# Optimization experiments

Measured on AMD Instinct MI355X. Metric: run time of the kernel, lower is better.

The kernel has to match this reference:

```python
import jax, jax.numpy as jnp
import numpy as np

D_MODEL = 1024
N_HEADS = 16
D_K = D_MODEL // N_HEADS  # 64
D_FF = 2688
THETA = 10000.0
EPS = 1e-5
B, S = 2, 2048


def _rmsnorm(x, w):
    xf = x.astype(jnp.float32)
    ms = jnp.mean(xf * xf, axis=-1, keepdims=True)
    return (xf * w * jax.lax.rsqrt(ms + EPS)).astype(x.dtype)


def _rope(x, cos, sin):
    # x: [B, S, H, D_K]; cos/sin: [S, D_K//2]
    xe = x[..., 0::2]
    xo = x[..., 1::2]
    c = cos[None, :, None, :]
    s = sin[None, :, None, :]
    re = xe * c - xo * s
    ro = xe * s + xo * c
    # interleave back to even/odd layout
    return jnp.stack([re, ro], axis=-1).reshape(x.shape)


def setup_inputs() -> dict:
    key = jax.random.key(0)
    ks = jax.random.split(key, 12)
    sc = 0.02  # keep activations numerically sane (stand-in for trunc_normal init)
    return {
        "x": jax.random.normal(ks[0], (B, S, D_MODEL), dtype=jnp.float32),
        "ln1_w": jax.random.normal(ks[1], (D_MODEL,), dtype=jnp.float32) * sc + 1.0,
        "q_w": jax.random.normal(ks[2], (D_MODEL, D_MODEL), dtype=jnp.float32) * sc,
        "k_w": jax.random.normal(ks[3], (D_MODEL, D_MODEL), dtype=jnp.float32) * sc,
        "v_w": jax.random.normal(ks[4], (D_MODEL, D_MODEL), dtype=jnp.float32) * sc,
        "o_w": jax.random.normal(ks[5], (D_MODEL, D_MODEL), dtype=jnp.float32) * sc,
        "ln2_w": jax.random.normal(ks[6], (D_MODEL,), dtype=jnp.float32) * sc + 1.0,
        "w1_w": jax.random.normal(ks[7], (D_FF, D_MODEL), dtype=jnp.float32) * sc,
        "w3_w": jax.random.normal(ks[8], (D_FF, D_MODEL), dtype=jnp.float32) * sc,
        "w2_w": jax.random.normal(ks[9], (D_MODEL, D_FF), dtype=jnp.float32) * sc,
        "token_positions": jnp.arange(S, dtype=jnp.int32),
    }


def reference(x, ln1_w, q_w, k_w, v_w, o_w, ln2_w, w1_w, w3_w, w2_w, token_positions):
    b, s, _ = x.shape
    # --- pre-norm attention sublayer ---
    h = _rmsnorm(x, ln1_w)
    Q = (h @ q_w.T).reshape(b, s, N_HEADS, D_K)
    K = (h @ k_w.T).reshape(b, s, N_HEADS, D_K)
    V = (h @ v_w.T).reshape(b, s, N_HEADS, D_K)

    # RoPE tables from token positions
    pos = token_positions.astype(jnp.float32)                      # [S]
    kk = jnp.arange(D_K // 2, dtype=jnp.float32)
    inv_freq = THETA ** (-2.0 * kk / D_K)                          # [D_K/2]
    ang = pos[:, None] * inv_freq[None, :]                          # [S, D_K/2]
    cos, sin = jnp.cos(ang), jnp.sin(ang)

    Qr = _rope(Q, cos, sin)
    Kr = _rope(K, cos, sin)

    scale = 1.0 / jnp.sqrt(jnp.float32(D_K))
    scores = jnp.einsum("bqhd,bkhd->bhqk", Qr, Kr) * scale          # [B,H,S,S]
    causal = jnp.tril(jnp.ones((s, s), dtype=bool))
    scores = jnp.where(causal[None, None], scores, jnp.float32(-10000.0))
    attn = jax.nn.softmax(scores, axis=-1)
    ctx = jnp.einsum("bhqk,bkhd->bqhd", attn, V).reshape(b, s, D_MODEL)
    x1 = x + ctx @ o_w.T

    # --- pre-norm SwiGLU FFN sublayer ---
    h2 = _rmsnorm(x1, ln2_w)
    g = h2 @ w1_w.T                                                 # [B,S,D_FF]
    u = h2 @ w3_w.T
    ffn = (g * jax.nn.sigmoid(g) * u) @ w2_w.T
    return x1 + ffn
```

## Files before the change

kernel.cpp:

```cpp
#include <hip/hip_runtime.h>
#include <cstdint>

#define DM   1024
#define NH   16
#define DK   64
#define DFF  2688
#define SEQ  2048
#define BB   2
#define MTOT (BB*SEQ)

typedef __attribute__((ext_vector_type(8))) short short8;
typedef __attribute__((ext_vector_type(4))) float f32x4;

typedef const __attribute__((address_space(1))) void* gaddr_t;
typedef __attribute__((address_space(3))) void* laddr_t;
#define GLOAD_LDS16(g, l) __builtin_amdgcn_global_load_lds((gaddr_t)(g), (laddr_t)(l), 16, 0, 0)
#define MFMA16(a, b, c) __builtin_amdgcn_mfma_f32_16x16x32_bf16((a), (b), (c), 0, 0, 0)
#define WAIT_LDS() __builtin_amdgcn_s_waitcnt(0xc07f)

#define VMCNT(n) asm volatile("s_waitcnt vmcnt(" #n ")" ::: "memory")
#define BAR() do { asm volatile("" ::: "memory"); \
                   __builtin_amdgcn_s_barrier();  \
                   asm volatile("" ::: "memory"); } while (0)

__device__ __forceinline__ float bf2f(unsigned short u) {
    union { unsigned int i; float f; } v; v.i = ((unsigned int)u) << 16; return v.f;
}
__device__ __forceinline__ unsigned short f2bf(float f) {
    union { float f; unsigned int i; } v; v.f = f;
    unsigned int r = v.i + 0x7fffu + ((v.i >> 16) & 1u);
    return (unsigned short)(r >> 16);
}
__device__ __forceinline__ unsigned long long pack4bf(float a, float b, float c, float d) {
    return (unsigned long long)f2bf(a) | ((unsigned long long)f2bf(b) << 16)
         | ((unsigned long long)f2bf(c) << 32) | ((unsigned long long)f2bf(d) << 48);
}

__global__ __launch_bounds__(256)
void prologue_k(const float* __restrict__ q_w, const float* __restrict__ k_w,
                const float* __restrict__ v_w, const float* __restrict__ o_w,
                const float* __restrict__ w1_w, const float* __restrict__ w3_w,
                const float* __restrict__ w2_w,
                unsigned short* __restrict__ Wqkv, unsigned short* __restrict__ Wo,
                unsigned short* __restrict__ W13, unsigned short* __restrict__ W2,
                const int* __restrict__ pos, float* __restrict__ tab,
                const float* __restrict__ x, const float* __restrict__ ln1_w,
                unsigned short* __restrict__ H) {
    const int blk = blockIdx.x;
    const int tid = threadIdx.x;
    if (blk < 12160) {
        const float* src; unsigned short* dst; int cols, rmul, roff, i;
        if (blk < 4096) {
            const int rr = blk >> 10;
            i = (blk & 1023) * 256 + tid;
            cols = 1024; rmul = 1;
            if (rr == 0)      { src = q_w; dst = Wqkv; roff = 0; }
            else if (rr == 1) { src = k_w; dst = Wqkv; roff = 1024; }
            else if (rr == 2) { src = v_w; dst = Wqkv; roff = 2048; }
            else              { src = o_w; dst = Wo;   roff = 0; }
        } else if (blk < 6784) {
            i = (blk - 4096) * 256 + tid; src = w1_w; dst = W13; cols = 1024; rmul = 2; roff = 0;
        } else if (blk < 9472) {
            i = (blk - 6784) * 256 + tid; src = w3_w; dst = W13; cols = 1024; rmul = 2; roff = 1;
        } else {
            i = (blk - 9472) * 256 + tid; src = w2_w; dst = W2;  cols = 2688; rmul = 1; roff = 0;
        }
        const int e = i * 4;
        const int r = e / cols, c = e - r * cols;
        const float4 v = *(const float4*)(src + e);
        ushort4 o;
        o.x = f2bf(v.x); o.y = f2bf(v.y); o.z = f2bf(v.z); o.w = f2bf(v.w);
        *(ushort4*)(dst + (size_t)(r * rmul + roff) * cols + c) = o;
    } else if (blk < 12672) {
        const int s = (blk - 12160) * 4 + (tid >> 6);
        const int t = tid & 63;
        const int kk = t & 31;
        const float ang = (float)pos[s] * __expf(-0.28782313662f * (float)kk);
        tab[s * 64 + t] = (t < 32) ? cosf(ang) : sinf(ang);
    } else {
        const int row = blk - 12672;
        const float4 v = ((const float4*)(x + (size_t)row * DM))[tid];
        float ss = v.x * v.x + v.y * v.y + v.z * v.z + v.w * v.w;
#pragma unroll
        for (int off = 32; off > 0; off >>= 1) ss += __shfl_down(ss, off, 64);
        __shared__ float sred[4];
        const int wave = tid >> 6, lane = tid & 63;
        if (lane == 0) sred[wave] = ss;
        __syncthreads();
        const float tot = sred[0] + sred[1] + sred[2] + sred[3];
        const float rinv = rsqrtf(tot * (1.0f / DM) + 1e-5f);
        const float4 wv = ((const float4*)ln1_w)[tid];
        ushort4 o;
        o.x = f2bf(v.x * wv.x * rinv);
        o.y = f2bf(v.y * wv.y * rinv);
        o.z = f2bf(v.z * wv.z * rinv);
        o.w = f2bf(v.w * wv.w * rinv);
        ((ushort4*)(H + (size_t)row * DM))[tid] = o;
    }
}

__global__ __launch_bounds__(256)
void rmsnorm_k(const float* __restrict__ x, const float* __restrict__ w,
               unsigned short* __restrict__ out) {
    const int row = blockIdx.x;
    const int tid = threadIdx.x;
    const float4 v = ((const float4*)(x + (size_t)row * DM))[tid];
    float ss = v.x * v.x + v.y * v.y + v.z * v.z + v.w * v.w;
#pragma unroll
    for (int off = 32; off > 0; off >>= 1) ss += __shfl_down(ss, off, 64);
    __shared__ float sred[4];
    const int wave = tid >> 6, lane = tid & 63;
    if (lane == 0) sred[wave] = ss;
    __syncthreads();
    const float tot = sred[0] + sred[1] + sred[2] + sred[3];
    const float rinv = rsqrtf(tot * (1.0f / DM) + 1e-5f);
    const float4 wv = ((const float4*)w)[tid];
    ushort4 o;
    o.x = f2bf(v.x * wv.x * rinv);
    o.y = f2bf(v.y * wv.y * rinv);
    o.z = f2bf(v.z * wv.z * rinv);
    o.w = f2bf(v.w * wv.w * rinv);
    ((ushort4*)(out + (size_t)row * DM))[tid] = o;
}

template <int EPI>
__global__ __launch_bounds__(512)
void gemm256(const unsigned short* __restrict__ A,
             const unsigned short* __restrict__ B,
             unsigned short* __restrict__ O0,
             unsigned short* __restrict__ O1,
             unsigned short* __restrict__ O2,
             const float* __restrict__ ROPT,
             int N, int K) {
    __shared__ unsigned short As[2][16384];
    __shared__ unsigned short Bs[2][12288];
    const int tid = threadIdx.x;
    const int wave = tid >> 6, lane = tid & 63;
    const int l15 = lane & 15, quad = lane >> 4;

    const int gx = gridDim.x;
    const int nwg = gx * gridDim.y;
    const int lin = blockIdx.y * gx + blockIdx.x;
    const int swz = (lin & 7) * (nwg >> 3) + (lin >> 3);
    const int bx = swz % gx, by = swz / gx;
    const int m0 = by * 256, n0 = bx * 192;
    const int wr = (wave >> 2) * 128, wc = (wave & 3) * 48;

    const f32x4 z4 = {0.f, 0.f, 0.f, 0.f};
    f32x4 acc[8][3];
#pragma unroll
    for (int m = 0; m < 8; m++)
#pragma unroll
        for (int n = 0; n < 3; n++) acc[m][n] = z4;

    const unsigned short* pa[4];
    int la[4];
#pragma unroll
    for (int r = 0; r < 4; r++) {
        const int s = r * 512 + tid;
        pa[r] = A + (size_t)(m0 + (s & 255)) * K + (s >> 8) * 8;
        la[r] = (r * 512 + wave * 64) * 8;
    }
    const unsigned short* pb[3];
    int lb[3];
#pragma unroll
    for (int r = 0; r < 3; r++) {
        const int s = r * 512 + tid;
        const int bk = s / 192, br = s - bk * 192;
        pb[r] = B + (size_t)(n0 + br) * K + bk * 8;
        lb[r] = (r * 512 + wave * 64) * 8;
    }

    const int nt = K >> 6;

#pragma unroll
    for (int r = 0; r < 4; r++) { GLOAD_LDS16(pa[r], &As[0][la[r]]); pa[r] += 64; }
#pragma unroll
    for (int r = 0; r < 3; r++) { GLOAD_LDS16(pb[r], &Bs[0][lb[r]]); pb[r] += 64; }

    int cur = 0;
    for (int t = 0; t < nt; ++t) {
        const int nb = cur ^ 1;
        if (t + 1 < nt) {
#pragma unroll
            for (int r = 0; r < 4; r++) { GLOAD_LDS16(pa[r], &As[nb][la[r]]); pa[r] += 64; }
            VMCNT(4);
        } else {
            VMCNT(0);
        }
        BAR();

        short8 bg[3][2];
#pragma unroll
        for (int n = 0; n < 3; n++)
#pragma unroll
            for (int kk = 0; kk < 2; kk++)
                bg[n][kk] = *(const short8*)(&Bs[cur][((quad + 4 * kk) * 192 + wc + n * 16 + l15) * 8]);

        short8 afA[2][2], afB[2][2];
#pragma unroll
        for (int m = 0; m < 2; m++)
#pragma unroll
            for (int kk = 0; kk < 2; kk++)
                afA[m][kk] = *(const short8*)(&As[cur][((quad + 4 * kk) * 256 + wr + m * 16 + l15) * 8]);

#pragma unroll
        for (int p = 0; p < 4; ++p) {
            short8 (&afC)[2][2] = (p & 1) ? afB : afA;
            short8 (&afN)[2][2] = (p & 1) ? afA : afB;
            if (p < 3) {
#pragma unroll
                for (int m = 0; m < 2; m++)
#pragma unroll
                    for (int kk = 0; kk < 2; kk++)
                        afN[m][kk] = *(const short8*)(&As[cur][((quad + 4 * kk) * 256 + wr + ((p + 1) * 2 + m) * 16 + l15) * 8]);
            }
            if (p == 1 && t + 1 < nt) {
#pragma unroll
                for (int r = 0; r < 3; r++) { GLOAD_LDS16(pb[r], &Bs[nb][lb[r]]); pb[r] += 64; }
            }
            __builtin_amdgcn_s_setprio(1);
#pragma unroll
            for (int m = 0; m < 2; m++)
#pragma unroll
                for (int n = 0; n < 3; n++)
#pragma unroll
                    for (int kk = 0; kk < 2; kk++)
                        acc[p * 2 + m][n] = MFMA16(bg[n][kk], afC[m][kk], acc[p * 2 + m][n]);
            __builtin_amdgcn_s_setprio(0);
            BAR();
        }
        cur = nb;
    }

#pragma unroll
    for (int m = 0; m < 8; m++) {
        const int r = m0 + wr + m * 16 + l15;
        if (EPI == 0) {
            const int b = r >> 11, s = r & (SEQ - 1);
            const float* rt = ROPT + s * 64;
#pragma unroll
            for (int n = 0; n < 3; n++) {
                const int cb = n0 + wc + n * 16;
                const int sec = cb >> 10;
                const int h = (cb & 1023) >> 6;
                const int cc0 = (cb & 63) + quad * 4;
                const f32x4 a = acc[m][n];
                if (sec < 2) {
                    const int p0 = cc0 >> 1;
                    const float cA = rt[p0],     sA = rt[32 + p0];
                    const float cB = rt[p0 + 1], sB = rt[32 + p0 + 1];
                    const float e0 = a[0] * cA - a[1] * sA;
                    const float o0 = a[0] * sA + a[1] * cA;
                    const float e1 = a[2] * cB - a[3] * sB;
                    const float o1 = a[2] * sB + a[3] * cB;
                    unsigned short* dst = (sec == 0) ? O0 : O1;
                    *(unsigned long long*)(dst + ((size_t)(b * NH + h) * SEQ + s) * DK + cc0) =
                        pack4bf(e0, o0, e1, o1);
                } else {
                    unsigned short* dst = O2 + ((size_t)(b * NH + h) * DK) * SEQ + s;
#pragma unroll
                    for (int tq = 0; tq < 4; tq++)
                        dst[(size_t)(cc0 + tq) * SEQ] = f2bf(a[tq]);
                }
            }
        } else {
#pragma unroll
            for (int n = 0; n < 3; n++) {
                const int cc = n0 + wc + n * 16 + quad * 4;
                const f32x4 a = acc[m][n];
                const float s1 = a[0] * a[1] / (1.f + __expf(-a[0]));
                const float s2 = a[2] * a[3] / (1.f + __expf(-a[2]));
                *(unsigned int*)(O0 + (size_t)r * (DFF) + (cc >> 1)) =
                    (unsigned int)f2bf(s1) | ((unsigned int)f2bf(s2) << 16);
            }
        }
    }
}

__global__ __launch_bounds__(512)
void gemm_thin(const unsigned short* __restrict__ A,
               const unsigned short* __restrict__ B,
               float* __restrict__ Cf,
               const float* __restrict__ R,
               int N, int K) {
    __shared__ unsigned short As[2][8192];
    __shared__ unsigned short Bs[2][8192];
    const int tid = threadIdx.x;
    const int wave = tid >> 6, lane = tid & 63;
    const int l15 = lane & 15, quad = lane >> 4;

    const int gx = gridDim.x;
    const int nwg = gx * gridDim.y;
    const int lin = blockIdx.y * gx + blockIdx.x;
    const int swz = (lin & 7) * (nwg >> 3) + (lin >> 3);
    const int bx = swz % gx, by = swz / gx;
    const int m0 = by * 128, n0 = bx * 128;
    const int wr = (wave >> 2) * 64, wc = (wave & 3) * 32;

    const f32x4 z4 = {0.f, 0.f, 0.f, 0.f};
    f32x4 acc[4][2];
#pragma unroll
    for (int m = 0; m < 4; m++)
#pragma unroll
        for (int n = 0; n < 2; n++) acc[m][n] = z4;

    const unsigned short* pa[2];
    const unsigned short* pb[2];
    int la[2], lb[2];
#pragma unroll
    for (int r = 0; r < 2; r++) {
        const int s = r * 512 + tid;
        pa[r] = A + (size_t)(m0 + (s & 127)) * K + (s >> 7) * 8;
        pb[r] = B + (size_t)(n0 + (s & 127)) * K + (s >> 7) * 8;
        la[r] = (r * 512 + wave * 64) * 8;
        lb[r] = la[r];
    }

    const int nt = K >> 6;

#pragma unroll
    for (int r = 0; r < 2; r++) { GLOAD_LDS16(pa[r], &As[0][la[r]]); pa[r] += 64; }
#pragma unroll
    for (int r = 0; r < 2; r++) { GLOAD_LDS16(pb[r], &Bs[0][lb[r]]); pb[r] += 64; }

    int cur = 0;
    for (int t = 0; t < nt; ++t) {
        const int nb = cur ^ 1;
        if (t + 1 < nt) {
#pragma unroll
            for (int r = 0; r < 2; r++) { GLOAD_LDS16(pa[r], &As[nb][la[r]]); pa[r] += 64; }
            VMCNT(2);
        } else {
            VMCNT(0);
        }
        BAR();

        short8 bg[2][2];
#pragma unroll
        for (int n = 0; n < 2; n++)
#pragma unroll
            for (int kk = 0; kk < 2; kk++)
                bg[n][kk] = *(const short8*)(&Bs[cur][((quad + 4 * kk) * 128 + wc + n * 16 + l15) * 8]);

#pragma unroll
        for (int p = 0; p < 2; ++p) {
            if (p == 0 && t + 1 < nt) {
#pragma unroll
                for (int r = 0; r < 2; r++) { GLOAD_LDS16(pb[r], &Bs[nb][lb[r]]); pb[r] += 64; }
            }
            short8 af[2][2];
#pragma unroll
            for (int m = 0; m < 2; m++)
#pragma unroll
                for (int kk = 0; kk < 2; kk++)
                    af[m][kk] = *(const short8*)(&As[cur][((quad + 4 * kk) * 128 + wr + (p * 2 + m) * 16 + l15) * 8]);
            __builtin_amdgcn_s_setprio(1);
#pragma unroll
            for (int m = 0; m < 2; m++)
#pragma unroll
                for (int n = 0; n < 2; n++)
#pragma unroll
                    for (int kk = 0; kk < 2; kk++)
                        acc[p * 2 + m][n] = MFMA16(bg[n][kk], af[m][kk], acc[p * 2 + m][n]);
            __builtin_amdgcn_s_setprio(0);
            BAR();
        }
        cur = nb;
    }

#pragma unroll
    for (int i = 0; i < 4; i++) {
        const int r = m0 + wr + i * 16 + l15;
#pragma unroll
        for (int j = 0; j < 2; j++) {
            const int cc = n0 + wc + j * 16 + quad * 4;
            const size_t idx = (size_t)r * N + cc;
            const float4 rv = *(const float4*)(R + idx);
            float4 ov;
            ov.x = acc[i][j][0] + rv.x;
            ov.y = acc[i][j][1] + rv.y;
            ov.z = acc[i][j][2] + rv.z;
            ov.w = acc[i][j][3] + rv.w;
            *(float4*)(Cf + idx) = ov;
        }
    }
}

template <bool MASK>
__device__ __forceinline__ void softmax_tile(f32x4 st[4], float& li, unsigned short* Pw,
                                             int l15, int quad, int j0, int myq) {
    float lsum = 0.f;
#pragma unroll
    for (int t = 0; t < 4; t++) {
#pragma unroll
        for (int r = 0; r < 4; r++) {
            float v = st[t][r] * 0.125f;
            if (MASK) {
                const int key = j0 + t * 16 + quad * 4 + r;
                if (key > myq) v = -1e30f;
            }
            const float p = __expf(v);
            st[t][r] = p;
            lsum += p;
        }
        *(unsigned long long*)(Pw + l15 * 72 + t * 16 + quad * 4) =
            pack4bf(st[t][0], st[t][1], st[t][2], st[t][3]);
    }
    li += lsum;
}

__global__ __launch_bounds__(256, 2)
void attn_k(const unsigned short* __restrict__ Qr, const unsigned short* __restrict__ Kr,
            const unsigned short* __restrict__ Vt, unsigned short* __restrict__ ctx) {
    __shared__ unsigned short KVl[2][8192];
    __shared__ unsigned short Pl[4 * 2 * 1152];
    const int tid = threadIdx.x;
    const int wave = tid >> 6, lane = tid & 63;
    const int l15 = lane & 15, quad = lane >> 4;
    const int bh = blockIdx.y, b = bh >> 4, h = bh & 15;
    const int g = blockIdx.x;
    const int qtA = g * 4 + wave, qtB = 127 - qtA;
    const int q0A = qtA * 16, q0B = qtB * 16;
    const int countA = g + 1, countB = 32 - g;
    const unsigned short* Kb = Kr + (size_t)bh * SEQ * DK;
    const unsigned short* Vb = Vt + (size_t)bh * DK * SEQ;

    const unsigned short* QbA = Qr + ((size_t)bh * SEQ + q0A) * DK;
    const unsigned short* QbB = Qr + ((size_t)bh * SEQ + q0B) * DK;
    const short8 qfA0 = *(const short8*)(QbA + l15 * DK + quad * 8);
    const short8 qfA1 = *(const short8*)(QbA + l15 * DK + 32 + quad * 8);
    const short8 qfB0 = *(const short8*)(QbB + l15 * DK + quad * 8);
    const short8 qfB1 = *(const short8*)(QbB + l15 * DK + 32 + quad * 8);

    const int slot0 = wave * 128 + lane, slot1 = slot0 + 64;
    const int ck0 = slot0 >> 3, s0 = slot0 & 7;
    const int ck1 = slot1 >> 3, s1 = slot1 & 7;
    const unsigned short* kp0 = Kb + ck0 * 64 + (s0 ^ (ck0 & 7)) * 8;
    const unsigned short* kp1 = Kb + ck1 * 64 + (s1 ^ (ck1 & 7)) * 8;
    const unsigned short* vp0 = Vb + ck0 * 2048 + (s0 ^ (ck0 & 7)) * 8;
    const unsigned short* vp1 = Vb + ck1 * 2048 + (s1 ^ (ck1 & 7)) * 8;
    const int kb0 = wave * 1024, kb1 = kb0 + 512;

    unsigned short* PA = Pl + (wave * 2 + 0) * 1152;
    unsigned short* PB = Pl + (wave * 2 + 1) * 1152;

    const f32x4 z4 = {0.f, 0.f, 0.f, 0.f};
    f32x4 oA[4], oB[4];
#pragma unroll
    for (int d = 0; d < 4; d++) { oA[d] = z4; oB[d] = z4; }
    float liA = 0.f, liB = 0.f;
    const int myqA = q0A + l15, myqB = q0B + l15;
    const int xr = l15 & 7;

    GLOAD_LDS16(kp0, &KVl[0][kb0]);
    GLOAD_LDS16(kp1, &KVl[0][kb1]);
    GLOAD_LDS16(vp0, &KVl[0][4096 + kb0]);
    GLOAD_LDS16(vp1, &KVl[0][4096 + kb1]);
    kp0 += 4096; kp1 += 4096; vp0 += 64; vp1 += 64;

    for (int j = 0; j < countB; ++j) {
        const int bf = j & 1;
        const unsigned short* Kl = KVl[bf];
        const unsigned short* Vl = KVl[bf] + 4096;
        __syncthreads();
        if (j + 1 < countB) {
            GLOAD_LDS16(kp0, &KVl[bf ^ 1][kb0]);
            GLOAD_LDS16(kp1, &KVl[bf ^ 1][kb1]);
            GLOAD_LDS16(vp0, &KVl[bf ^ 1][4096 + kb0]);
            GLOAD_LDS16(vp1, &KVl[bf ^ 1][4096 + kb1]);
            kp0 += 4096; kp1 += 4096; vp0 += 64; vp1 += 64;
        }
        const int j0 = j * 64;
        short8 kf[4][2];
#pragma unroll
        for (int t = 0; t < 4; t++) {
            const unsigned short* kr = Kl + (t * 16 + l15) * 64;
            kf[t][0] = *(const short8*)(kr + (quad ^ xr) * 8);
            kf[t][1] = *(const short8*)(kr + ((4 + quad) ^ xr) * 8);
        }
        f32x4 stB[4];
        __builtin_amdgcn_s_setprio(1);
#pragma unroll
        for (int t = 0; t < 4; t++)
            stB[t] = MFMA16(kf[t][1], qfB1, MFMA16(kf[t][0], qfB0, z4));
        __builtin_amdgcn_s_setprio(0);
        const bool doA = (j < countA);
        if (doA) {
            f32x4 stA[4];
            __builtin_amdgcn_s_setprio(1);
#pragma unroll
            for (int t = 0; t < 4; t++)
                stA[t] = MFMA16(kf[t][1], qfA1, MFMA16(kf[t][0], qfA0, z4));
            __builtin_amdgcn_s_setprio(0);
            if (j == countA - 1) softmax_tile<true >(stA, liA, PA, l15, quad, j0, myqA);
            else                 softmax_tile<false>(stA, liA, PA, l15, quad, j0, myqA);
        }
        if (j == countB - 1) softmax_tile<true >(stB, liB, PB, l15, quad, j0, myqB);
        else                 softmax_tile<false>(stB, liB, PB, l15, quad, j0, myqB);
        WAIT_LDS();
        short8 vf[4][2];
#pragma unroll
        for (int dt = 0; dt < 4; dt++) {
            const unsigned short* vr = Vl + (dt * 16 + l15) * 64;
            vf[dt][0] = *(const short8*)(vr + (quad ^ xr) * 8);
            vf[dt][1] = *(const short8*)(vr + ((4 + quad) ^ xr) * 8);
        }
        {
            const short8 pfB0 = *(const short8*)(PB + l15 * 72 + quad * 8);
            const short8 pfB1 = *(const short8*)(PB + l15 * 72 + 32 + quad * 8);
            __builtin_amdgcn_s_setprio(1);
#pragma unroll
            for (int dt = 0; dt < 4; dt++)
                oB[dt] = MFMA16(vf[dt][1], pfB1, MFMA16(vf[dt][0], pfB0, oB[dt]));
            __builtin_amdgcn_s_setprio(0);
        }
        if (doA) {
            const short8 pfA0 = *(const short8*)(PA + l15 * 72 + quad * 8);
            const short8 pfA1 = *(const short8*)(PA + l15 * 72 + 32 + quad * 8);
            __builtin_amdgcn_s_setprio(1);
#pragma unroll
            for (int dt = 0; dt < 4; dt++)
                oA[dt] = MFMA16(vf[dt][1], pfA1, MFMA16(vf[dt][0], pfA0, oA[dt]));
            __builtin_amdgcn_s_setprio(0);
        }
    }
    liA += __shfl_xor(liA, 16, 64); liA += __shfl_xor(liA, 32, 64);
    liB += __shfl_xor(liB, 16, 64); liB += __shfl_xor(liB, 32, 64);
    const float invA = 1.0f / liA, invB = 1.0f / liB;
#pragma unroll
    for (int dt = 0; dt < 4; dt++) {
        *(unsigned long long*)(PA + l15 * 72 + dt * 16 + quad * 4) =
            pack4bf(oA[dt][0] * invA, oA[dt][1] * invA, oA[dt][2] * invA, oA[dt][3] * invA);
        *(unsigned long long*)(PB + l15 * 72 + dt * 16 + quad * 4) =
            pack4bf(oB[dt][0] * invB, oB[dt][1] * invB, oB[dt][2] * invB, oB[dt][3] * invB);
    }
    WAIT_LDS();
    const int row = lane >> 2, seg = (lane & 3) * 8;
#pragma unroll
    for (int p = 0; p < 2; p++) {
        const int cs = seg + p * 32;
        const uint4 va = *(const uint4*)(PA + row * 72 + cs);
        *(uint4*)(ctx + ((size_t)b * SEQ + q0A + row) * DM + h * DK + cs) = va;
        const uint4 vb = *(const uint4*)(PB + row * 72 + cs);
        *(uint4*)(ctx + ((size_t)b * SEQ + q0B + row) * DM + h * DK + cs) = vb;
    }
}

extern "C" void kernel_launch(void* const* d_in, const int* in_sizes, int n_in,
                              void* d_out, int out_size, void* d_ws, size_t ws_size,
                              hipStream_t stream) {
    const float* x     = (const float*)d_in[0];
    const float* ln1_w = (const float*)d_in[1];
    const float* q_w   = (const float*)d_in[2];
    const float* k_w   = (const float*)d_in[3];
    const float* v_w   = (const float*)d_in[4];
    const float* o_w   = (const float*)d_in[5];
    const float* ln2_w = (const float*)d_in[6];
    const float* w1_w  = (const float*)d_in[7];
    const float* w3_w  = (const float*)d_in[8];
    const float* w2_w  = (const float*)d_in[9];
    const int*   tpos  = (const int*)d_in[10];
    float* out = (float*)d_out;
    char* ws = (char*)d_ws;

    unsigned short* Wqkv = (unsigned short*)(ws + 0);
    unsigned short* Wo   = (unsigned short*)(ws + 6291456);
    unsigned short* W13  = (unsigned short*)(ws + 8388608);
    unsigned short* W2   = (unsigned short*)(ws + 19398656);
    float*          X1   = (float*)(ws + 24903680);
    float*          ROPT = (float*)(ws + 24903680);
    char* base = ws + 41680896;
    unsigned short* H    = (unsigned short*)(base);
    unsigned short* QR   = (unsigned short*)(base + 8388608);
    unsigned short* KR   = (unsigned short*)(base + 16777216);
    unsigned short* VT   = (unsigned short*)(base + 25165824);
    unsigned short* CTX  = (unsigned short*)(base + 33554432);
    unsigned short* H2   = (unsigned short*)(base);
    unsigned short* ACT  = (unsigned short*)(base + 41943040);

    prologue_k<<<16768, 256, 0, stream>>>(q_w, k_w, v_w, o_w, w1_w, w3_w, w2_w,
                                          Wqkv, Wo, W13, W2, tpos, ROPT,
                                          x, ln1_w, H);
    gemm256<0><<<dim3(16, 16), 512, 0, stream>>>(H, Wqkv, QR, KR, VT, ROPT, 3072, 1024);
    attn_k<<<dim3(16, 32), 256, 0, stream>>>(QR, KR, VT, CTX);
    gemm_thin<<<dim3(8, 32), 512, 0, stream>>>(CTX, Wo, X1, x, 1024, 1024);
    rmsnorm_k<<<4096, 256, 0, stream>>>(X1, ln2_w, H2);
    gemm256<1><<<dim3(28, 16), 512, 0, stream>>>(H2, W13, ACT, nullptr, nullptr, nullptr, 5376, 1024);
    gemm_thin<<<dim3(8, 32), 512, 0, stream>>>(ACT, W2, out, X1, 1024, 2688);
}
```

Before: 391.7 us.

## Use a 256x384 output tile for the fused W1/W3 SwiGLU GEMM

Adds a dedicated gemm384 kernel with 256x384 tiles (8 waves, each computing 128x96) for the W1/W3 projection with the SwiGLU epilogue, launched on a 14x16 grid instead of a 28x16 grid of 256x192 tiles. The larger N tile raises arithmetic intensity per loaded A tile and halves the number of workgroups. In exchange it uses more LDS (80KB double-buffered) and more accumulator registers, and leaves 224 workgroups, which may underfill the 256 CUs. The old EPI==1 path is removed from gemm256.

```diff
diff --git a/kernel.cpp b/kernel.cpp
--- a/kernel.cpp
+++ b/kernel.cpp
@@ -236,44 +236,139 @@
 #pragma unroll
     for (int m = 0; m < 8; m++) {
         const int r = m0 + wr + m * 16 + l15;
-        if (EPI == 0) {
-            const int b = r >> 11, s = r & (SEQ - 1);
-            const float* rt = ROPT + s * 64;
-#pragma unroll
-            for (int n = 0; n < 3; n++) {
-                const int cb = n0 + wc + n * 16;
-                const int sec = cb >> 10;
-                const int h = (cb & 1023) >> 6;
-                const int cc0 = (cb & 63) + quad * 4;
-                const f32x4 a = acc[m][n];
-                if (sec < 2) {
-                    const int p0 = cc0 >> 1;
-                    const float cA = rt[p0],     sA = rt[32 + p0];
-                    const float cB = rt[p0 + 1], sB = rt[32 + p0 + 1];
-                    const float e0 = a[0] * cA - a[1] * sA;
-                    const float o0 = a[0] * sA + a[1] * cA;
-                    const float e1 = a[2] * cB - a[3] * sB;
-                    const float o1 = a[2] * sB + a[3] * cB;
-                    unsigned short* dst = (sec == 0) ? O0 : O1;
-                    *(unsigned long long*)(dst + ((size_t)(b * NH + h) * SEQ + s) * DK + cc0) =
-                        pack4bf(e0, o0, e1, o1);
-                } else {
-                    unsigned short* dst = O2 + ((size_t)(b * NH + h) * DK) * SEQ + s;
-#pragma unroll
-                    for (int tq = 0; tq < 4; tq++)
-                        dst[(size_t)(cc0 + tq) * SEQ] = f2bf(a[tq]);
+        const int b = r >> 11, s = r & (SEQ - 1);
+        const float* rt = ROPT + s * 64;
+#pragma unroll
+        for (int n = 0; n < 3; n++) {
+            const int cb = n0 + wc + n * 16;
+            const int sec = cb >> 10;
+            const int h = (cb & 1023) >> 6;
+            const int cc0 = (cb & 63) + quad * 4;
+            const f32x4 a = acc[m][n];
+            if (sec < 2) {
+                const int p0 = cc0 >> 1;
+                const float cA = rt[p0],     sA = rt[32 + p0];
+                const float cB = rt[p0 + 1], sB = rt[32 + p0 + 1];
+                const float e0 = a[0] * cA - a[1] * sA;
+                const float o0 = a[0] * sA + a[1] * cA;
+                const float e1 = a[2] * cB - a[3] * sB;
+                const float o1 = a[2] * sB + a[3] * cB;
+                unsigned short* dst = (sec == 0) ? O0 : O1;
+                *(unsigned long long*)(dst + ((size_t)(b * NH + h) * SEQ + s) * DK + cc0) =
+                    pack4bf(e0, o0, e1, o1);
+            } else {
+                unsigned short* dst = O2 + ((size_t)(b * NH + h) * DK) * SEQ + s;
+#pragma unroll
+                for (int tq = 0; tq < 4; tq++)
+                    dst[(size_t)(cc0 + tq) * SEQ] = f2bf(a[tq]);
+            }
+        }
+    }
+}
+
+__global__ __launch_bounds__(512)
+void gemm384(const unsigned short* __restrict__ A,
+             const unsigned short* __restrict__ B,
+             unsigned short* __restrict__ O0,
+             int N, int K) {
+    __shared__ unsigned short As[2][16384];
+    __shared__ unsigned short Bs[2][24576];
+    const int tid = threadIdx.x;
+    const int wave = tid >> 6, lane = tid & 63;
+    const int l15 = lane & 15, quad = lane >> 4;
+
+    const int gx = gridDim.x;
+    const int nwg = gx * gridDim.y;
+    const int lin = blockIdx.y * gx + blockIdx.x;
+    const int swz = (lin & 7) * (nwg >> 3) + (lin >> 3);
+    const int bx = swz % gx, by = swz / gx;
+    const int m0 = by * 256, n0 = bx * 384;
+    const int wr = (wave >> 2) * 128, wc = (wave & 3) * 96;
+
+    const f32x4 z4 = {0.f, 0.f, 0.f, 0.f};
+    f32x4 acc[8][6];
+#pragma unroll
+    for (int m = 0; m < 8; m++)
+#pragma unroll
+        for (int n = 0; n < 6; n++) acc[m][n] = z4;
+
+    const unsigned short* pa[4];
+    int la[4];
+#pragma unroll
+    for (int r = 0; r < 4; r++) {
+        const int s = r * 512 + tid;
+        pa[r] = A + (size_t)(m0 + (s & 255)) * K + (s >> 8) * 8;
+        la[r] = (r * 512 + wave * 64) * 8;
+    }
+    const unsigned short* pb[6];
+    int lb[6];
+#pragma unroll
+    for (int r = 0; r < 6; r++) {
+        const int s = r * 512 + tid;
+        const int bk = s / 384, br = s - bk * 384;
+        pb[r] = B + (size_t)(n0 + br) * K + bk * 8;
+        lb[r] = (r * 512 + wave * 64) * 8;
+    }
+
+    const int nt = K >> 6;
+
+#pragma unroll
+    for (int r = 0; r < 4; r++) { GLOAD_LDS16(pa[r], &As[0][la[r]]); pa[r] += 64; }
+#pragma unroll
+    for (int r = 0; r < 6; r++) { GLOAD_LDS16(pb[r], &Bs[0][lb[r]]); pb[r] += 64; }
+
+    int cur = 0;
+    for (int t = 0; t < nt; ++t) {
+        const int nb = cur ^ 1;
+        if (t + 1 < nt) {
+#pragma unroll
+            for (int r = 0; r < 4; r++) { GLOAD_LDS16(pa[r], &As[nb][la[r]]); pa[r] += 64; }
+            VMCNT(4);
+        } else {
+            VMCNT(0);
+        }
+        BAR();
+
+#pragma unroll
+        for (int p = 0; p < 4; ++p) {
+            if (p == 1 && t + 1 < nt) {
+#pragma unroll
+                for (int r = 0; r < 6; r++) { GLOAD_LDS16(pb[r], &Bs[nb][lb[r]]); pb[r] += 64; }
+            }
+            short8 af[2][2];
+#pragma unroll
+            for (int m = 0; m < 2; m++)
+#pragma unroll
+                for (int kk = 0; kk < 2; kk++)
+                    af[m][kk] = *(const short8*)(&As[cur][((quad + 4 * kk) * 256 + wr + (p * 2 + m) * 16 + l15) * 8]);
+            __builtin_amdgcn_s_setprio(1);
+#pragma unroll
+            for (int n = 0; n < 6; n++) {
+                short8 bg0 = *(const short8*)(&Bs[cur][((quad + 0) * 384 + wc + n * 16 + l15) * 8]);
+                short8 bg1 = *(const short8*)(&Bs[cur][((quad + 4) * 384 + wc + n * 16 + l15) * 8]);
+#pragma unroll
+                for (int m = 0; m < 2; m++) {
+                    acc[p * 2 + m][n] = MFMA16(bg0, af[m][0], acc[p * 2 + m][n]);
+                    acc[p * 2 + m][n] = MFMA16(bg1, af[m][1], acc[p * 2 + m][n]);
                 }
             }
-        } else {
-#pragma unroll
-            for (int n = 0; n < 3; n++) {
-                const int cc = n0 + wc + n * 16 + quad * 4;
-                const f32x4 a = acc[m][n];
-                const float s1 = a[0] * a[1] / (1.f + __expf(-a[0]));
-                const float s2 = a[2] * a[3] / (1.f + __expf(-a[2]));
-                *(unsigned int*)(O0 + (size_t)r * (DFF) + (cc >> 1)) =
-                    (unsigned int)f2bf(s1) | ((unsigned int)f2bf(s2) << 16);
-            }
+            __builtin_amdgcn_s_setprio(0);
+            BAR();
+        }
+        cur = nb;
+    }
+
+#pragma unroll
+    for (int m = 0; m < 8; m++) {
+        const int r = m0 + wr + m * 16 + l15;
+#pragma unroll
+        for (int n = 0; n < 6; n++) {
+            const int cc = n0 + wc + n * 16 + quad * 4;
+            const f32x4 a = acc[m][n];
+            const float s1 = a[0] * a[1] / (1.f + __expf(-a[0]));
+            const float s2 = a[2] * a[3] / (1.f + __expf(-a[2]));
+            *(unsigned int*)(O0 + (size_t)r * (DFF) + (cc >> 1)) =
+                (unsigned int)f2bf(s1) | ((unsigned int)f2bf(s2) << 16);
         }
     }
 }
@@ -586,6 +681,6 @@
     attn_k<<<dim3(16, 32), 256, 0, stream>>>(QR, KR, VT, CTX);
     gemm_thin<<<dim3(8, 32), 512, 0, stream>>>(CTX, Wo, X1, x, 1024, 1024);
     rmsnorm_k<<<4096, 256, 0, stream>>>(X1, ln2_w, H2);
-    gemm256<1><<<dim3(28, 16), 512, 0, stream>>>(H2, W13, ACT, nullptr, nullptr, nullptr, 5376, 1024);
+    gemm384<<<dim3(14, 16), 512, 0, stream>>>(H2, W13, ACT, 5376, 1024);
     gemm_thin<<<dim3(8, 32), 512, 0, stream>>>(ACT, W2, out, X1, 1024, 2688);
 }
```

Measured after the change: 438.7 us. +12.0%, slower.
